# Optimization experiments

Hardware: AMD Instinct MI355X
Metric: run time of the kernel (lower is better)

The kernel has to match this reference:

```python
import jax, jax.numpy as jnp
import numpy as np
import math

B, T, C, H, RANK, RD = 8, 512, 2048, 16, 8, 16
HD = C // H  # 128
ADAPTER_SCALE = 1.0 / RANK  # scale / rank with scale=1.0


def setup_inputs() -> dict:
    key = jax.random.key(0)
    ks = jax.random.split(key, 7)
    x = jax.random.normal(ks[0], (B, T, C), dtype=jnp.float32)
    # frozen random linears (weights ~ N(0,1)/sqrt(in_features))
    Wqkv = jax.random.normal(ks[1], (3 * C, C), dtype=jnp.float32) / math.sqrt(C)
    Wout = jax.random.normal(ks[2], (C, C), dtype=jnp.float32) / math.sqrt(C)
    # VeRA frozen random matrices
    A0_qkv = jax.random.normal(ks[3], (RANK, C), dtype=jnp.float32) / math.sqrt(C)
    B0_qkv = jax.random.normal(ks[4], (3 * C, RANK), dtype=jnp.float32) / math.sqrt(RANK)
    A0_out = jax.random.normal(ks[5], (RANK, C), dtype=jnp.float32) / math.sqrt(C)
    B0_out = jax.random.normal(ks[6], (C, RANK), dtype=jnp.float32) / math.sqrt(RANK)
    # learned scaling vectors (init to ones, as in the module)
    d_a_qkv = jnp.ones((RANK,), dtype=jnp.float32)
    d_b_qkv = jnp.ones((RANK,), dtype=jnp.float32)
    d_a_out = jnp.ones((RANK,), dtype=jnp.float32)
    d_b_out = jnp.ones((RANK,), dtype=jnp.float32)
    # partial RoPE caches over first RD dims
    freqs = 1.0 / (10000.0 ** (jnp.arange(0, RD, 2, dtype=jnp.float32) / RD))  # [RD/2]
    ang = jnp.arange(T, dtype=jnp.float32)[:, None] * freqs[None, :]  # [T, RD/2]
    cos = jnp.cos(ang)
    sin = jnp.sin(ang)
    return {"x": x, "Wqkv": Wqkv, "A0_qkv": A0_qkv, "B0_qkv": B0_qkv,
            "d_a_qkv": d_a_qkv, "d_b_qkv": d_b_qkv,
            "Wout": Wout, "A0_out": A0_out, "B0_out": B0_out,
            "d_a_out": d_a_out, "d_b_out": d_b_out,
            "cos": cos, "sin": sin}


def _adapted_linear(x, W, A0, B0, d_a, d_b):
    # frozen(x) + VeRA adapter: diag(d_b) B0 diag(d_a) A0, scaled by 1/rank
    base = x @ W.T
    h = (x @ A0.T) * (d_a * d_b)
    return base + (h @ B0.T) * ADAPTER_SCALE


def _apply_rope(q, cos, sin):
    # q: [B, H, T, HD]; rotate first RD dims, pass-through the rest
    x_rope, x_pass = q[..., :RD], q[..., RD:]
    half = RD // 2
    x1, x2 = x_rope[..., :half], x_rope[..., half:]
    c = cos[None, None]  # [1,1,T,RD/2]
    s = sin[None, None]
    rot = jnp.concatenate([x1 * c - x2 * s, x2 * c + x1 * s], axis=-1)
    return jnp.concatenate([rot, x_pass], axis=-1)


def reference(x, Wqkv, A0_qkv, B0_qkv, d_a_qkv, d_b_qkv,
              Wout, A0_out, B0_out, d_a_out, d_b_out, cos, sin):
    qkv = _adapted_linear(x, Wqkv, A0_qkv, B0_qkv, d_a_qkv, d_b_qkv)  # [B,T,3C]
    qkv = qkv.reshape(B, T, 3, H, HD)
    q = jnp.transpose(qkv[:, :, 0], (0, 2, 1, 3))  # [B,H,T,HD]
    k = jnp.transpose(qkv[:, :, 1], (0, 2, 1, 3))
    v = jnp.transpose(qkv[:, :, 2], (0, 2, 1, 3))
    q = _apply_rope(q, cos, sin)
    k = _apply_rope(k, cos, sin)
    # causal SDPA
    scale = 1.0 / math.sqrt(HD)
    scores = jnp.einsum('bhqd,bhkd->bhqk', q, k) * scale
    mask = jnp.tril(jnp.ones((T, T), dtype=bool))
    scores = jnp.where(mask[None, None], scores, jnp.finfo(scores.dtype).min)
    attn = jax.nn.softmax(scores, axis=-1)
    y = jnp.einsum('bhqk,bhkd->bhqd', attn, v)  # [B,H,T,HD]
    y = jnp.transpose(y, (0, 2, 1, 3)).reshape(B, T, C)
    return _adapted_linear(y, Wout, A0_out, B0_out, d_a_out, d_b_out)
```

## Files before the change

kernel.cpp:

```cpp
#include <hip/hip_runtime.h>

typedef unsigned short ushort_t;
typedef __attribute__((ext_vector_type(8))) short short8;
typedef __attribute__((ext_vector_type(4))) float f32x4;

#define AS1(p) ((const __attribute__((address_space(1))) void*)(p))
#define AS3(p) ((__attribute__((address_space(3))) void*)(p))

__device__ __forceinline__ ushort_t f2bf(float f){
  unsigned u = __float_as_uint(f);
  u += 0x7FFFu + ((u>>16)&1u);
  return (ushort_t)(u>>16);
}
__device__ __forceinline__ float bf2f(ushort_t h){
  return __uint_as_float(((unsigned)h)<<16);
}

__global__ __launch_bounds__(256) void conv_f2b(const float* __restrict__ src,
                                                ushort_t* __restrict__ dst, int n){
  int i = (blockIdx.x*256 + threadIdx.x)*4;
  if (i < n){
    float4 v = *(const float4*)&src[i];
    ushort_t o0=f2bf(v.x), o1=f2bf(v.y), o2=f2bf(v.z), o3=f2bf(v.w);
    ushort4 o; o.x=o0; o.y=o1; o.z=o2; o.w=o3;
    *(ushort4*)&dst[i] = o;
  }
}

__global__ __launch_bounds__(256) void lora_h_f32(const float* __restrict__ X,
                                                  ushort_t* __restrict__ Xbf,
                                                  const float* __restrict__ A0,
                                                  const float* __restrict__ da,
                                                  const float* __restrict__ db,
                                                  float* __restrict__ out, int K){
  int m = blockIdx.x;
  int tid = threadIdx.x, lane = tid & 63, w = tid >> 6;
  float part[8] = {0,0,0,0,0,0,0,0};
  for (int k = tid; k < K; k += 256){
    float xv = X[(size_t)m*K + k];
    Xbf[(size_t)m*K + k] = f2bf(xv);
    #pragma unroll
    for (int r=0;r<8;++r) part[r] += xv * A0[r*K + k];
  }
  #pragma unroll
  for (int r=0;r<8;++r)
    for (int d=1;d<64;d<<=1) part[r] += __shfl_xor(part[r], d, 64);
  __shared__ float wsum[4][8];
  if (lane==0){
    #pragma unroll
    for (int r=0;r<8;++r) wsum[w][r] = part[r];
  }
  __syncthreads();
  if (tid < 8){
    float s = wsum[0][tid]+wsum[1][tid]+wsum[2][tid]+wsum[3][tid];
    out[(size_t)m*8 + tid] = s * da[tid]*db[tid];
  }
}

__global__ __launch_bounds__(256) void lora_h_bf16(const ushort_t* __restrict__ X,
                                                   const float* __restrict__ A0,
                                                   const float* __restrict__ da,
                                                   const float* __restrict__ db,
                                                   float* __restrict__ out, int K){
  int m = blockIdx.x;
  int tid = threadIdx.x, lane = tid & 63, w = tid >> 6;
  float part[8] = {0,0,0,0,0,0,0,0};
  for (int k = tid; k < K; k += 256){
    float xv = bf2f(X[(size_t)m*K + k]);
    #pragma unroll
    for (int r=0;r<8;++r) part[r] += xv * A0[r*K + k];
  }
  #pragma unroll
  for (int r=0;r<8;++r)
    for (int d=1;d<64;d<<=1) part[r] += __shfl_xor(part[r], d, 64);
  __shared__ float wsum[4][8];
  if (lane==0){
    #pragma unroll
    for (int r=0;r<8;++r) wsum[w][r] = part[r];
  }
  __syncthreads();
  if (tid < 8){
    float s = wsum[0][tid]+wsum[1][tid]+wsum[2][tid]+wsum[3][tid];
    out[(size_t)m*8 + tid] = s * da[tid]*db[tid];
  }
}

__global__ __launch_bounds__(512, 1) void gemm256x192_lora(
    const ushort_t* __restrict__ A, const ushort_t* __restrict__ Bw,
    const float* __restrict__ hmat, const float* __restrict__ B0,
    ushort_t* __restrict__ C, int M, int N, int K)
{
  __shared__ __align__(16) char smem[114688];
  const int tid = threadIdx.x, lane = tid & 63, w = tid >> 6;
  const int wm = w >> 1, wn = w & 1;

  const int nbn = N / 192;
  const int nwg = (M >> 8) * nbn;
  const int q8 = nwg >> 3;
  const int swz = ((int)blockIdx.x & 7)*q8 + ((int)blockIdx.x >> 3);
  const int m0 = (swz / nbn) << 8, n0 = (swz % nbn) * 192;

  const int NTt = K >> 6;
  const int srow8  = tid >> 3;
  const int schunk = (lane & 7) ^ (lane >> 3);

  #define STAGE_AU(u, tt, bb) do { \
    const ushort_t* g_ = A + (size_t)(m0 + (u)*64 + srow8)*K + (tt)*64 + schunk*8; \
    __builtin_amdgcn_global_load_lds(AS1(g_), AS3(smem + (bb)*32768 + (u)*8192 + tid*16), 16, 0, 0); \
  } while(0)
  #define STAGE_BU(u, tt, bb) do { \
    const ushort_t* g_ = Bw + (size_t)(n0 + (u)*64 + srow8)*K + (tt)*64 + schunk*8; \
    __builtin_amdgcn_global_load_lds(AS1(g_), AS3(smem + 65536 + (bb)*24576 + (u)*8192 + tid*16), 16, 0, 0); \
  } while(0)

  #define RDA(bb, q, kk) (*(const short8*)(smem + (bb)*32768 + \
      ((q)*64 + wm*16 + (lane&15))*128 + ((((kk)*4 + (lane>>4)) ^ (lane&7))<<4)))
  #define RDB(bb, r, kk) (*(const short8*)(smem + 65536 + (bb)*24576 + \
      ((r)*32 + wn*16 + (lane&15))*128 + ((((kk)*4 + (lane>>4)) ^ (lane&7))<<4)))

  #define MM(q, r, bi) do{ \
    acc[q][r] = __builtin_amdgcn_mfma_f32_16x16x32_bf16(aF[q][0], bF[bi][0], acc[q][r], 0,0,0); \
    acc[q][r] = __builtin_amdgcn_mfma_f32_16x16x32_bf16(aF[q][1], bF[bi][1], acc[q][r], 0,0,0); \
  }while(0)

  #define BARRIER() asm volatile("s_barrier" ::: "memory")

  short8 aF[4][2];
  short8 bF[2][2];
  f32x4 acc[4][6] = {};

  STAGE_AU(0,0,0); STAGE_AU(1,0,0); STAGE_AU(2,0,0); STAGE_AU(3,0,0);
  STAGE_BU(0,0,0); STAGE_BU(1,0,0); STAGE_BU(2,0,0);
  asm volatile("s_waitcnt vmcnt(2)" ::: "memory");
  BARRIER();

  for (int t = 0; t < NTt-1; ++t){
    const int b = t & 1, nb = b ^ 1;
    #pragma unroll
    for (int q=0;q<4;++q){ aF[q][0]=RDA(b,q,0); aF[q][1]=RDA(b,q,1); }
    #pragma unroll
    for (int rl=0;rl<2;++rl){ bF[rl][0]=RDB(b,rl,0); bF[rl][1]=RDB(b,rl,1); }
    STAGE_AU(0,t+1,nb); STAGE_AU(1,t+1,nb);
    __builtin_amdgcn_s_setprio(1);
    MM(0,0,0); MM(0,1,1); MM(1,0,0); MM(1,1,1);
    MM(2,0,0); MM(2,1,1); MM(3,0,0); MM(3,1,1);
    __builtin_amdgcn_s_setprio(0);
    asm volatile("s_waitcnt vmcnt(3)" ::: "memory");
    BARRIER();
    #pragma unroll
    for (int rl=0;rl<2;++rl){ bF[rl][0]=RDB(b,rl+2,0); bF[rl][1]=RDB(b,rl+2,1); }
    STAGE_AU(2,t+1,nb); STAGE_AU(3,t+1,nb); STAGE_BU(0,t+1,nb);
    __builtin_amdgcn_s_setprio(1);
    MM(0,2,0); MM(0,3,1); MM(1,2,0); MM(1,3,1);
    MM(2,2,0); MM(2,3,1); MM(3,2,0); MM(3,3,1);
    __builtin_amdgcn_s_setprio(0);
    asm volatile("s_waitcnt vmcnt(5)" ::: "memory");
    BARRIER();
    #pragma unroll
    for (int rl=0;rl<2;++rl){ bF[rl][0]=RDB(b,rl+4,0); bF[rl][1]=RDB(b,rl+4,1); }
    STAGE_BU(1,t+1,nb); STAGE_BU(2,t+1,nb);
    __builtin_amdgcn_s_setprio(1);
    MM(0,4,0); MM(0,5,1); MM(1,4,0); MM(1,5,1);
    MM(2,4,0); MM(2,5,1); MM(3,4,0); MM(3,5,1);
    __builtin_amdgcn_s_setprio(0);
    asm volatile("s_waitcnt lgkmcnt(0)" ::: "memory");
    asm volatile("s_waitcnt vmcnt(2)" ::: "memory");
    BARRIER();
  }

  {
    const int b = (NTt-1) & 1;
    #pragma unroll
    for (int q=0;q<4;++q){ aF[q][0]=RDA(b,q,0); aF[q][1]=RDA(b,q,1); }
    #pragma unroll
    for (int rl=0;rl<2;++rl){ bF[rl][0]=RDB(b,rl,0); bF[rl][1]=RDB(b,rl,1); }
    __builtin_amdgcn_s_setprio(1);
    MM(0,0,0); MM(0,1,1); MM(1,0,0); MM(1,1,1);
    MM(2,0,0); MM(2,1,1); MM(3,0,0); MM(3,1,1);
    __builtin_amdgcn_s_setprio(0);
    asm volatile("s_waitcnt vmcnt(1)" ::: "memory");
    BARRIER();
    #pragma unroll
    for (int rl=0;rl<2;++rl){ bF[rl][0]=RDB(b,rl+2,0); bF[rl][1]=RDB(b,rl+2,1); }
    __builtin_amdgcn_s_setprio(1);
    MM(0,2,0); MM(0,3,1); MM(1,2,0); MM(1,3,1);
    MM(2,2,0); MM(2,3,1); MM(3,2,0); MM(3,3,1);
    __builtin_amdgcn_s_setprio(0);
    asm volatile("s_waitcnt vmcnt(0)" ::: "memory");
    BARRIER();
    #pragma unroll
    for (int rl=0;rl<2;++rl){ bF[rl][0]=RDB(b,rl+4,0); bF[rl][1]=RDB(b,rl+4,1); }
    MM(0,4,0); MM(0,5,1); MM(1,4,0); MM(1,5,1);
    MM(2,4,0); MM(2,5,1); MM(3,4,0); MM(3,5,1);
  }

  float b0v[6][8];
  #pragma unroll
  for (int r=0;r<6;++r){
    int col = n0 + r*32 + wn*16 + (lane&15);
    const float4* bp = (const float4*)&B0[(size_t)col*8];
    float4 u0 = bp[0], u1 = bp[1];
    b0v[r][0]=u0.x; b0v[r][1]=u0.y; b0v[r][2]=u0.z; b0v[r][3]=u0.w;
    b0v[r][4]=u1.x; b0v[r][5]=u1.y; b0v[r][6]=u1.z; b0v[r][7]=u1.w;
  }
  #pragma unroll
  for (int q=0;q<4;++q){
    #pragma unroll
    for (int jj=0;jj<4;++jj){
      int row = m0 + q*64 + wm*16 + (lane>>4)*4 + jj;
      const float4* hp = (const float4*)&hmat[(size_t)row*8];
      float4 h0 = hp[0], h1 = hp[1];
      #pragma unroll
      for (int r=0;r<6;++r){
        float lor = h0.x*b0v[r][0]+h0.y*b0v[r][1]+h0.z*b0v[r][2]+h0.w*b0v[r][3]
                  + h1.x*b0v[r][4]+h1.y*b0v[r][5]+h1.z*b0v[r][6]+h1.w*b0v[r][7];
        int col = n0 + r*32 + wn*16 + (lane&15);
        C[(size_t)row*N + col] = f2bf(acc[q][r][jj] + 0.125f*lor);
      }
    }
  }
  #undef STAGE_AU
  #undef STAGE_BU
  #undef RDA
  #undef RDB
  #undef MM
  #undef BARRIER
}

template<int MODE>
__global__ __launch_bounds__(512, 1) void gemm128x256_lora(
    const ushort_t* __restrict__ A, const ushort_t* __restrict__ Bw,
    const float* __restrict__ hmat, const float* __restrict__ B0,
    void* __restrict__ C, int M, int N, int K)
{
  __shared__ __align__(16) char smem[98304];
  const int tid = threadIdx.x, lane = tid & 63, w = tid >> 6;
  const int wm = w >> 2, wn = w & 3;

  const int nbn = N >> 8;
  const int nwg = (M >> 7) * nbn;
  const int q8 = nwg >> 3;
  const int swz = ((int)blockIdx.x & 7)*q8 + ((int)blockIdx.x >> 3);
  const int m0 = (swz / nbn) << 7, n0 = (swz % nbn) << 8;

  const int NTt = K >> 6;

  const int srow8  = tid >> 3;
  const int schunk = (lane & 7) ^ (lane >> 3);

  #define STAGE_AU(u, tt, bb) do { \
    const ushort_t* g_ = A + (size_t)(m0 + (u)*64 + srow8)*K + (tt)*64 + schunk*8; \
    __builtin_amdgcn_global_load_lds(AS1(g_), AS3(smem + (bb)*16384 + (u)*8192 + w*1024), 16, 0, 0); \
  } while(0)
  #define STAGE_BU(u, tt, bb) do { \
    const ushort_t* g_ = Bw + (size_t)(n0 + (u)*64 + srow8)*K + (tt)*64 + schunk*8; \
    __builtin_amdgcn_global_load_lds(AS1(g_), AS3(smem + 32768 + (bb)*32768 + (u)*8192 + w*1024), 16, 0, 0); \
  } while(0)

  #define RDA(bb, q, kk) (*(const short8*)(smem + (bb)*16384 + \
      ((q)*32 + wm*16 + (lane&15))*128 + ((((kk)*4 + (lane>>4)) ^ (lane&7))<<4)))
  #define RDB(bb, rg, kk) (*(const short8*)(smem + 32768 + (bb)*32768 + \
      ((rg)*64 + wn*16 + (lane&15))*128 + ((((kk)*4 + (lane>>4)) ^ (lane&7))<<4)))

  #define MM0(q,rl) do{ \
    acc[q][rl] = __builtin_amdgcn_mfma_f32_16x16x32_bf16(aF[q][0], bF[rl][0], acc[q][rl], 0,0,0); \
    acc[q][rl] = __builtin_amdgcn_mfma_f32_16x16x32_bf16(aF[q][1], bF[rl][1], acc[q][rl], 0,0,0); \
  }while(0)
  #define MM1(q,rl) do{ \
    acc[q][(rl)+2] = __builtin_amdgcn_mfma_f32_16x16x32_bf16(aF[q][0], bF[rl][0], acc[q][(rl)+2], 0,0,0); \
    acc[q][(rl)+2] = __builtin_amdgcn_mfma_f32_16x16x32_bf16(aF[q][1], bF[rl][1], acc[q][(rl)+2], 0,0,0); \
  }while(0)

  #define BARRIER() asm volatile("s_barrier" ::: "memory")

  short8 aF[4][2];
  short8 bF[2][2];
  f32x4 acc[4][4] = {};

  STAGE_AU(0,0,0); STAGE_AU(1,0,0); STAGE_BU(0,0,0); STAGE_BU(1,0,0);
  STAGE_BU(2,0,0); STAGE_BU(3,0,0);
  asm volatile("s_waitcnt vmcnt(2)" ::: "memory");
  BARRIER();

  for (int t = 0; t < NTt-1; ++t){
    const int b = t & 1, nb = b ^ 1;
    #pragma unroll
    for (int q=0;q<4;++q){ aF[q][0]=RDA(b,q,0); aF[q][1]=RDA(b,q,1); }
    #pragma unroll
    for (int rl=0;rl<2;++rl){ bF[rl][0]=RDB(b,rl,0); bF[rl][1]=RDB(b,rl,1); }
    STAGE_AU(0,t+1,nb); STAGE_AU(1,t+1,nb); STAGE_BU(0,t+1,nb); STAGE_BU(1,t+1,nb);
    __builtin_amdgcn_s_setprio(1);
    MM0(0,0); MM0(0,1); MM0(1,0); MM0(1,1);
    MM0(2,0); MM0(2,1); MM0(3,0); MM0(3,1);
    __builtin_amdgcn_s_setprio(0);
    asm volatile("s_waitcnt vmcnt(4)" ::: "memory");
    BARRIER();
    #pragma unroll
    for (int rl=0;rl<2;++rl){ bF[rl][0]=RDB(b,rl+2,0); bF[rl][1]=RDB(b,rl+2,1); }
    STAGE_BU(2,t+1,nb); STAGE_BU(3,t+1,nb);
    __builtin_amdgcn_s_setprio(1);
    MM1(0,0); MM1(0,1); MM1(1,0); MM1(1,1);
    MM1(2,0); MM1(2,1); MM1(3,0); MM1(3,1);
    __builtin_amdgcn_s_setprio(0);
    asm volatile("s_waitcnt lgkmcnt(0)" ::: "memory");
    asm volatile("s_waitcnt vmcnt(2)" ::: "memory");
    BARRIER();
  }

  {
    const int b = (NTt-1) & 1;
    #pragma unroll
    for (int q=0;q<4;++q){ aF[q][0]=RDA(b,q,0); aF[q][1]=RDA(b,q,1); }
    #pragma unroll
    for (int rl=0;rl<2;++rl){ bF[rl][0]=RDB(b,rl,0); bF[rl][1]=RDB(b,rl,1); }
    __builtin_amdgcn_s_setprio(1);
    MM0(0,0); MM0(0,1); MM0(1,0); MM0(1,1);
    MM0(2,0); MM0(2,1); MM0(3,0); MM0(3,1);
    __builtin_amdgcn_s_setprio(0);
    asm volatile("s_waitcnt vmcnt(0)" ::: "memory");
    BARRIER();
    #pragma unroll
    for (int rl=0;rl<2;++rl){ bF[rl][0]=RDB(b,rl+2,0); bF[rl][1]=RDB(b,rl+2,1); }
    MM1(0,0); MM1(0,1); MM1(1,0); MM1(1,1);
    MM1(2,0); MM1(2,1); MM1(3,0); MM1(3,1);
  }

  float b0v[4][8];
  #pragma unroll
  for (int r=0;r<4;++r){
    int col = n0 + r*64 + wn*16 + (lane&15);
    const float4* bp = (const float4*)&B0[(size_t)col*8];
    float4 u0 = bp[0], u1 = bp[1];
    b0v[r][0]=u0.x; b0v[r][1]=u0.y; b0v[r][2]=u0.z; b0v[r][3]=u0.w;
    b0v[r][4]=u1.x; b0v[r][5]=u1.y; b0v[r][6]=u1.z; b0v[r][7]=u1.w;
  }
  #pragma unroll
  for (int q=0;q<4;++q){
    #pragma unroll
    for (int jj=0;jj<4;++jj){
      int row = m0 + q*32 + wm*16 + (lane>>4)*4 + jj;
      const float4* hp = (const float4*)&hmat[(size_t)row*8];
      float4 h0 = hp[0], h1 = hp[1];
      #pragma unroll
      for (int r=0;r<4;++r){
        float lor = h0.x*b0v[r][0]+h0.y*b0v[r][1]+h0.z*b0v[r][2]+h0.w*b0v[r][3]
                  + h1.x*b0v[r][4]+h1.y*b0v[r][5]+h1.z*b0v[r][6]+h1.w*b0v[r][7];
        int col = n0 + r*64 + wn*16 + (lane&15);
        float v = acc[q][r][jj] + 0.125f*lor;
        if (MODE==0) ((ushort_t*)C)[(size_t)row*N + col] = f2bf(v);
        else         ((float*)C)[(size_t)row*N + col]    = v;
      }
    }
  }
  #undef STAGE_AU
  #undef STAGE_BU
  #undef RDA
  #undef RDB
  #undef MM0
  #undef MM1
  #undef BARRIER
}

__global__ __launch_bounds__(256) void rope_kernel(ushort_t* __restrict__ qkv,
                                                   const float* __restrict__ cosb,
                                                   const float* __restrict__ sinb){
  int idx = blockIdx.x*256 + threadIdx.x;
  int d = idx & 7;
  int g = idx >> 3;
  int h_ = g & 15;
  int s  = (g>>4) & 1;
  int t  = (g>>5) & 511;
  int b  = g >> 14;
  size_t base = (size_t)(b*512 + t)*6144 + s*2048 + h_*128;
  float x1 = bf2f(qkv[base+d]), x2 = bf2f(qkv[base+d+8]);
  float c = cosb[t*8+d], sn = sinb[t*8+d];
  qkv[base+d]   = f2bf(x1*c - x2*sn);
  qkv[base+d+8] = f2bf(x2*c + x1*sn);
}

__global__ __launch_bounds__(512) void attn_kernel(const ushort_t* __restrict__ qkv,
                                                   ushort_t* __restrict__ y){
  __shared__ __align__(16) ushort_t Ks[2][64*128];
  __shared__ __align__(16) ushort_t Vt[2][128*64];
  __shared__ __align__(16) ushort_t Pl[8][16*64];

  const int qt = blockIdx.x, hh = blockIdx.y, b = blockIdx.z;
  const int tid = threadIdx.x, lane = tid & 63, w = tid >> 6, g = lane >> 4;
  const int qb0 = qt*128;
  const int row_base = b*512;
  const int qoff = hh*128;
  const int koff = 2048 + hh*128;
  const int voff = 4096 + hh*128;
  const float scale = 0.08838834764831845f;

  short8 qf[4];
  {
    int qr = qb0 + w*16 + (lane & 15);
    const ushort_t* qp = qkv + (size_t)(row_base + qr)*6144 + qoff + g*8;
    #pragma unroll
    for (int kc=0;kc<4;++kc) qf[kc] = *(const short8*)(qp + kc*32);
  }

  const int krow = tid >> 4;
  const int kc_  = tid & 15;
  const int kcs  = (kc_ & 8) | ((kc_ ^ (krow & 7)) & 7);
  const int vr   = tid >> 3;
  const int vd0  = (tid & 7) * 16;
  const int vrhi = vr >> 3, vrlo = vr & 7;

  const int nt = 2*qt + 2;
  const int wmin = qb0 + w*16;
  const int wmax = wmin + 15;

  f32x4 o[8] = {};
  float mrow[4] = {-1e30f,-1e30f,-1e30f,-1e30f};
  float lrow[4] = {0,0,0,0};

  short8 vv0, vv1;

  {
    const ushort_t* kg = qkv + (size_t)(row_base + krow)*6144 + koff + kcs*8;
    __builtin_amdgcn_global_load_lds(AS1(kg), AS3((char*)&Ks[0][0] + tid*16), 16, 0, 0);
    __builtin_amdgcn_global_load_lds(AS1(kg + (size_t)32*6144), AS3((char*)&Ks[0][0] + 8192 + tid*16), 16, 0, 0);
    const ushort_t* vg = qkv + (size_t)(row_base + vr)*6144 + voff + vd0;
    vv0 = ((const short8*)vg)[0];
    vv1 = ((const short8*)vg)[1];
    #pragma unroll
    for (int ii=0;ii<8;++ii){
      int sw = (vrhi ^ ii) << 3;
      Vt[0][(vd0 + ii    )*64 + sw + vrlo] = (ushort_t)vv0[ii];
      Vt[0][(vd0 + 8 + ii)*64 + sw + vrlo] = (ushort_t)vv1[ii];
    }
  }
  __syncthreads();

  for (int t = 0; t < nt; ++t){
    const int bb = t & 1, nb = bb ^ 1;
    const int kv0 = t*64;
    const bool have_next = (t+1 < nt);

    if (have_next){
      const int kv1 = kv0 + 64;
      const ushort_t* kg = qkv + (size_t)(row_base + kv1 + krow)*6144 + koff + kcs*8;
      __builtin_amdgcn_global_load_lds(AS1(kg), AS3((char*)&Ks[nb][0] + tid*16), 16, 0, 0);
      __builtin_amdgcn_global_load_lds(AS1(kg + (size_t)32*6144), AS3((char*)&Ks[nb][0] + 8192 + tid*16), 16, 0, 0);
      const ushort_t* vg = qkv + (size_t)(row_base + kv1 + vr)*6144 + voff + vd0;
      vv0 = ((const short8*)vg)[0];
      vv1 = ((const short8*)vg)[1];
    }

    if (kv0 <= wmax){
      f32x4 s4[4] = {};
      #pragma unroll
      for (int cg=0;cg<4;++cg){
        const int row = cg*16 + (lane&15);
        const int rx = row & 7;
        #pragma unroll
        for (int kc=0;kc<4;++kc){
          const int ch = kc*4 + g;
          const short8 kfv = *(const short8*)&Ks[bb][row*128 + (((ch&8)|((ch^rx)&7))<<3)];
          s4[cg] = __builtin_amdgcn_mfma_f32_16x16x32_bf16(qf[kc], kfv, s4[cg], 0, 0, 0);
        }
      }

      const bool diag = (kv0 + 63 > wmin);
      float fac[4], p0[4], p1[4], p2[4], p3[4];
      #pragma unroll
      for (int j=0;j<4;++j){
        float a0 = s4[0][j]*scale, a1 = s4[1][j]*scale, a2 = s4[2][j]*scale, a3 = s4[3][j]*scale;
        if (diag){
          int q_abs = wmin + g*4 + j;
          int c0 = kv0 + (lane&15);
          if (c0      > q_abs) a0 = -1e30f;
          if (c0 + 16 > q_abs) a1 = -1e30f;
          if (c0 + 32 > q_abs) a2 = -1e30f;
          if (c0 + 48 > q_abs) a3 = -1e30f;
        }
        float mx = fmaxf(fmaxf(a0,a1), fmaxf(a2,a3));
        #pragma unroll
        for (int d=1; d<16; d<<=1) mx = fmaxf(mx, __shfl_xor(mx, d, 16));
        float mn = fmaxf(mrow[j], mx);
        float f  = __expf(mrow[j] - mn);
        mrow[j] = mn; fac[j] = f;
        p0[j] = __expf(a0 - mn); p1[j] = __expf(a1 - mn);
        p2[j] = __expf(a2 - mn); p3[j] = __expf(a3 - mn);
        float rs = p0[j] + p1[j] + p2[j] + p3[j];
        #pragma unroll
        for (int d=1; d<16; d<<=1) rs += __shfl_xor(rs, d, 16);
        lrow[j] = lrow[j]*f + rs;
      }
      #pragma unroll
      for (int n=0;n<8;++n){
        #pragma unroll
        for (int j=0;j<4;++j) o[n][j] *= fac[j];
      }

      {
        ushort_t* plw = &Pl[w][0];
        #pragma unroll
        for (int j=0;j<4;++j){
          const int prow = g*4 + j;
          const int rx = prow & 7;
          const int cl = (lane&15)>>3, c7 = lane&7;
          plw[prow*64 + (((0*2+cl)^rx)<<3) + c7] = f2bf(p0[j]);
          plw[prow*64 + (((1*2+cl)^rx)<<3) + c7] = f2bf(p1[j]);
          plw[prow*64 + (((2*2+cl)^rx)<<3) + c7] = f2bf(p2[j]);
          plw[prow*64 + (((3*2+cl)^rx)<<3) + c7] = f2bf(p3[j]);
        }
      }
      {
        const ushort_t* plw = &Pl[w][0];
        const int rowP = lane & 15, rxp = rowP & 7;
        const short8 pf0 = *(const short8*)&plw[rowP*64 + (((g  )^rxp)<<3)];
        const short8 pf1 = *(const short8*)&plw[rowP*64 + (((4+g)^rxp)<<3)];
        #pragma unroll
        for (int n=0;n<8;++n){
          const int d = n*16 + (lane&15);
          const int dx = d & 7;
          const short8 vf0 = *(const short8*)&Vt[bb][d*64 + (((g  )^dx)<<3)];
          const short8 vf1 = *(const short8*)&Vt[bb][d*64 + (((4+g)^dx)<<3)];
          o[n] = __builtin_amdgcn_mfma_f32_16x16x32_bf16(pf0, vf0, o[n], 0, 0, 0);
          o[n] = __builtin_amdgcn_mfma_f32_16x16x32_bf16(pf1, vf1, o[n], 0, 0, 0);
        }
      }
    }

    if (have_next){
      #pragma unroll
      for (int ii=0;ii<8;++ii){
        int sw = (vrhi ^ ii) << 3;
        Vt[nb][(vd0 + ii    )*64 + sw + vrlo] = (ushort_t)vv0[ii];
        Vt[nb][(vd0 + 8 + ii)*64 + sw + vrlo] = (ushort_t)vv1[ii];
      }
    }
    __syncthreads();
  }

  #pragma unroll
  for (int j=0;j<4;++j){
    float inv = 1.0f / lrow[j];
    int qr = qb0 + w*16 + g*4 + j;
    #pragma unroll
    for (int n=0;n<8;++n)
      y[(size_t)(row_base+qr)*2048 + hh*128 + n*16 + (lane&15)] = f2bf(o[n][j]*inv);
  }
}

extern "C" void kernel_launch(void* const* d_in, const int* in_sizes, int n_in,
                              void* d_out, int out_size, void* d_ws, size_t ws_size,
                              hipStream_t stream){
  const float* x       = (const float*)d_in[0];
  const float* Wqkv    = (const float*)d_in[1];
  const float* A0_qkv  = (const float*)d_in[2];
  const float* B0_qkv  = (const float*)d_in[3];
  const float* da_qkv  = (const float*)d_in[4];
  const float* db_qkv  = (const float*)d_in[5];
  const float* Wout    = (const float*)d_in[6];
  const float* A0_out  = (const float*)d_in[7];
  const float* B0_out  = (const float*)d_in[8];
  const float* da_out  = (const float*)d_in[9];
  const float* db_out  = (const float*)d_in[10];
  const float* cosb    = (const float*)d_in[11];
  const float* sinb    = (const float*)d_in[12];
  float* out = (float*)d_out;

  char* ws = (char*)d_ws;
  ushort_t* x_bf    = (ushort_t*)(ws);
  ushort_t* wqkv_bf = (ushort_t*)(ws + 16777216);
  ushort_t* wout_bf = (ushort_t*)(ws + 41943040);
  ushort_t* qkv_bf  = (ushort_t*)(ws + 50331648);
  ushort_t* y_bf    = (ushort_t*)(ws + 100663296);
  float*    h_qkv   = (float*)   (ws + 117440512);
  float*    h_out   = (float*)   (ws + 117571584);

  const int M = 4096;
  const int C = 2048;
  const int N3 = 6144;

  conv_f2b<<<12288,256, 0, stream>>>(Wqkv, wqkv_bf, N3*C);
  conv_f2b<<<4096, 256, 0, stream>>>(Wout, wout_bf, C*C);

  lora_h_f32<<<M, 256, 0, stream>>>(x, x_bf, A0_qkv, da_qkv, db_qkv, h_qkv, C);

  gemm256x192_lora<<<(M/256)*(N3/192), 512, 0, stream>>>(x_bf, wqkv_bf, h_qkv, B0_qkv,
                                                         qkv_bf, M, N3, C);

  rope_kernel<<<4096, 256, 0, stream>>>(qkv_bf, cosb, sinb);

  attn_kernel<<<dim3(4, 16, 8), 512, 0, stream>>>(qkv_bf, y_bf);

  lora_h_bf16<<<M, 256, 0, stream>>>(y_bf, A0_out, da_out, db_out, h_out, C);

  gemm128x256_lora<1><<<(M/128)*(C/256), 512, 0, stream>>>(y_bf, wout_bf, h_out, B0_out,
                                                           out, M, C, C);
}
```

Measured before the change: 248.3 us.

## Fuse RoPE into QKV GEMM epilogue and reorder attention block scheduling

Removes the standalone RoPE kernel and applies the rotation inside the QKV GEMM epilogue. Lanes swap their partner values with a cross-lane shuffle for columns that start a q or k head, which saves a launch and a read-modify-write pass over the qkv buffer. The attention launch also becomes a flat 1D grid with a remapped, interleaved order of query tiles, so that heavy and light causal tiles are spread more evenly across the device. The epilogue gains a branch and extra loads, and rounding now happens once after rotation instead of twice.

```diff
diff --git a/kernel.cpp b/kernel.cpp
--- a/kernel.cpp
+++ b/kernel.cpp
@@ -88,6 +88,7 @@
 __global__ __launch_bounds__(512, 1) void gemm256x192_lora(
     const ushort_t* __restrict__ A, const ushort_t* __restrict__ Bw,
     const float* __restrict__ hmat, const float* __restrict__ B0,
+    const float* __restrict__ cosb, const float* __restrict__ sinb,
     ushort_t* __restrict__ C, int M, int N, int K)
 {
   __shared__ __align__(16) char smem[114688];
@@ -214,8 +215,16 @@
       for (int r=0;r<6;++r){
         float lor = h0.x*b0v[r][0]+h0.y*b0v[r][1]+h0.z*b0v[r][2]+h0.w*b0v[r][3]
                   + h1.x*b0v[r][4]+h1.y*b0v[r][5]+h1.z*b0v[r][6]+h1.w*b0v[r][7];
-        int col = n0 + r*32 + wn*16 + (lane&15);
-        C[(size_t)row*N + col] = f2bf(acc[q][r][jj] + 0.125f*lor);
+        int colbase = n0 + r*32 + wn*16;
+        int col = colbase + (lane&15);
+        float v = acc[q][r][jj] + 0.125f*lor;
+        if ((colbase < 4096) && ((colbase & 127) == 0)){
+          float p = __shfl_xor(v, 8, 64);
+          int tt = row & 511, dd = lane & 7;
+          float cc = cosb[tt*8 + dd], ss = sinb[tt*8 + dd];
+          v = ((lane & 8) == 0) ? (v*cc - p*ss) : (v*cc + p*ss);
+        }
+        C[(size_t)row*N + col] = f2bf(v);
       }
     }
   }
@@ -361,30 +370,17 @@
   #undef BARRIER
 }
 
-__global__ __launch_bounds__(256) void rope_kernel(ushort_t* __restrict__ qkv,
-                                                   const float* __restrict__ cosb,
-                                                   const float* __restrict__ sinb){
-  int idx = blockIdx.x*256 + threadIdx.x;
-  int d = idx & 7;
-  int g = idx >> 3;
-  int h_ = g & 15;
-  int s  = (g>>4) & 1;
-  int t  = (g>>5) & 511;
-  int b  = g >> 14;
-  size_t base = (size_t)(b*512 + t)*6144 + s*2048 + h_*128;
-  float x1 = bf2f(qkv[base+d]), x2 = bf2f(qkv[base+d+8]);
-  float c = cosb[t*8+d], sn = sinb[t*8+d];
-  qkv[base+d]   = f2bf(x1*c - x2*sn);
-  qkv[base+d+8] = f2bf(x2*c + x1*sn);
-}
-
 __global__ __launch_bounds__(512) void attn_kernel(const ushort_t* __restrict__ qkv,
                                                    ushort_t* __restrict__ y){
   __shared__ __align__(16) ushort_t Ks[2][64*128];
   __shared__ __align__(16) ushort_t Vt[2][128*64];
   __shared__ __align__(16) ushort_t Pl[8][16*64];
 
-  const int qt = blockIdx.x, hh = blockIdx.y, b = blockIdx.z;
+  const int flat = blockIdx.x;
+  const int qt = ((flat >> 7) ^ ((flat >> 8) & 1)) & 3;
+  const int hb = flat & 127;
+  const int hh = hb & 15, b = hb >> 4;
+
   const int tid = threadIdx.x, lane = tid & 63, w = tid >> 6, g = lane >> 4;
   const int qb0 = qt*128;
   const int row_base = b*512;
@@ -583,11 +579,9 @@
   lora_h_f32<<<M, 256, 0, stream>>>(x, x_bf, A0_qkv, da_qkv, db_qkv, h_qkv, C);
 
   gemm256x192_lora<<<(M/256)*(N3/192), 512, 0, stream>>>(x_bf, wqkv_bf, h_qkv, B0_qkv,
-                                                         qkv_bf, M, N3, C);
-
-  rope_kernel<<<4096, 256, 0, stream>>>(qkv_bf, cosb, sinb);
-
-  attn_kernel<<<dim3(4, 16, 8), 512, 0, stream>>>(qkv_bf, y_bf);
+                                                         cosb, sinb, qkv_bf, M, N3, C);
+
+  attn_kernel<<<512, 512, 0, stream>>>(qkv_bf, y_bf);
 
   lora_h_bf16<<<M, 256, 0, stream>>>(y_bf, A0_out, da_out, db_out, h_out, C);
 
```

Measured after the change: 232.0 us. 6.6% less time.
